# Performance work log

Hardware: AMD Instinct MI355X
Metric: run time of the kernel (lower is better)

The kernel has to match this reference:

```python
import jax, jax.numpy as jnp
import numpy as np

TEMPERATURE = 100.0  # exponential-smoothing temperature from __init__ default
ETA = 1.0            # feature/label cost tradeoff


def _cdist(a, b):
    # Euclidean distance matrix [M, N] between rows of a [M, D] and b [N, D]
    sq = (jnp.sum(a * a, axis=1)[:, None]
          + jnp.sum(b * b, axis=1)[None, :]
          - 2.0 * (a @ b.T))
    return jnp.sqrt(jnp.maximum(sq, 1e-12))


def setup_inputs() -> dict:
    key = jax.random.key(0)
    ks = jax.random.split(key, 9)
    B, Nt, Ns, H, Wd, C = 1024, 8192, 8192, 32, 32, 10
    D = H * Wd
    x = jax.random.normal(ks[0], (B, H, Wd), jnp.float32)
    target_features = jax.random.normal(ks[1], (Nt, H, Wd), jnp.float32)
    aligned_source_features = jax.random.normal(ks[2], (Nt, H, Wd), jnp.float32)
    source_features = jax.random.normal(ks[3], (Ns, H, Wd), jnp.float32)
    source_high_dim_labels = jax.random.uniform(ks[4], (Ns, C), jnp.float32)
    aligned_target_labels = jax.random.uniform(ks[5], (Ns, C), jnp.float32)
    source_label_distances = jax.random.uniform(ks[6], (C, C), jnp.float32)
    W = jax.random.normal(ks[7], (D, C), jnp.float32) * 0.02
    b = jnp.zeros((C,), jnp.float32)
    return {
        "x": x,
        "target_features": target_features,
        "aligned_source_features": aligned_source_features,
        "source_features": source_features,
        "source_high_dim_labels": source_high_dim_labels,
        "aligned_target_labels": aligned_target_labels,
        "source_label_distances": source_label_distances,
        "W": W,
        "b": b,
    }


def reference(x, target_features, aligned_source_features, source_features,
              source_high_dim_labels, aligned_target_labels,
              source_label_distances, W, b):
    B = x.shape[0]
    xf = x.reshape(B, -1)                                   # [B, D]
    tf = target_features.reshape(target_features.shape[0], -1)       # [Nt, D]
    asf = aligned_source_features.reshape(aligned_source_features.shape[0], -1)  # [Nt, D]
    sf = source_features.reshape(source_features.shape[0], -1)       # [Ns, D]

    # --- feature transport: target -> source (plain_softmax) ---
    d_feat = _cdist(xf, tf)                                 # [B, Nt]
    w_feat = jax.nn.softmax(-TEMPERATURE * d_feat, axis=1)  # [B, Nt]
    x_src = w_feat @ asf                                    # [B, D] in source space

    # --- source model (linear classifier head -> soft predictions) ---
    preds = jax.nn.softmax(x_src @ W + b, axis=1)           # [B, C]

    # --- label transport: source -> target (plain_softmax) ---
    cost = _cdist(x_src, sf)                                # feature_dists=True: [B, Ns]
    # label_dists=True: cost of moving predicted label mass to each sample's label
    cost = cost + ETA * (preds @ source_label_distances @ source_high_dim_labels.T)
    w_lab = jax.nn.softmax(-TEMPERATURE * cost, axis=1)     # [B, Ns]
    y = w_lab @ aligned_target_labels                       # [B, C] in target label space
    return y
```

## Files before the change

### kernel.cpp

```cpp
#include <hip/hip_runtime.h>
#include <hip/hip_bf16.h>
#include <math.h>

#define B_ROWS 1024
#define NT 8192
#define NS 8192
#define DIM 1024
#define NC 10
#define TEMP 100.0f
#define WCAP 1024
#define CCAP 512
#define LTHR 18.421681f
#define PREP_RPB 8
#define TSTR 132

typedef __bf16 bf16x8 __attribute__((ext_vector_type(8)));
typedef __bf16 bf16x4 __attribute__((ext_vector_type(4)));
typedef float f32x4 __attribute__((ext_vector_type(4)));

#define GLOAD_LDS(g, l) \
    __builtin_amdgcn_global_load_lds((__attribute__((address_space(1))) void*)(g), \
                                     (__attribute__((address_space(3))) void*)(l), 16, 0, 0)

__device__ inline __bf16 split_hi(float v) { return (__bf16)v; }
__device__ inline __bf16 split_lo(float v) {
    __bf16 h = (__bf16)v;
    return (__bf16)(v - (float)h);
}

__device__ inline float wave_max(float v) {
    #pragma unroll
    for (int off = 32; off > 0; off >>= 1)
        v = fmaxf(v, __shfl_down(v, off, 64));
    return v;
}
__device__ inline float wave_sum(float v) {
    #pragma unroll
    for (int off = 32; off > 0; off >>= 1)
        v += __shfl_down(v, off, 64);
    return v;
}
__device__ inline float max4(float4 v) {
    return fmaxf(fmaxf(v.x, v.y), fmaxf(v.z, v.w));
}

__global__ __launch_bounds__(256) void k_prep0(const float* __restrict__ x,
                                               const float* __restrict__ tf,
                                               const float* __restrict__ sf,
                                               const float* __restrict__ sld,
                                               const float* __restrict__ shdl,
                                               const float* __restrict__ atl,
                                               __bf16* __restrict__ x2,
                                               __bf16* __restrict__ tf2,
                                               __bf16* __restrict__ sf2,
                                               float* __restrict__ nx_,
                                               float* __restrict__ nt_,
                                               float* __restrict__ ns_,
                                               float* __restrict__ M2Tt,
                                               float* __restrict__ atlt,
                                               int* __restrict__ cnt) {
    __shared__ float sred[4][PREP_RPB];
    __shared__ float sldL[NC * NC];
    const int NXB = B_ROWS / PREP_RPB;
    const int NTB = NT / PREP_RPB;
    const int NSB = NS / PREP_RPB;
    int b = blockIdx.x;
    int tid = threadIdx.x;
    if (b < NXB + NTB + NSB) {
        const float* Xp; __bf16* X2p; float* np; int r0;
        if (b < NXB)            { Xp = x;  X2p = x2;  np = nx_; r0 = b * PREP_RPB; }
        else if (b < NXB + NTB) { Xp = tf; X2p = tf2; np = nt_; r0 = (b - NXB) * PREP_RPB; }
        else                    { Xp = sf; X2p = sf2; np = ns_; r0 = (b - NXB - NTB) * PREP_RPB; }
        int c = tid * 4;
        int lane = tid & 63, wid = tid >> 6;
        #pragma unroll
        for (int r = 0; r < PREP_RPB; r++) {
            float4 v = *(const float4*)(Xp + (size_t)(r0 + r) * DIM + c);
            bf16x4 h, l;
            h[0] = split_hi(v.x); l[0] = split_lo(v.x);
            h[1] = split_hi(v.y); l[1] = split_lo(v.y);
            h[2] = split_hi(v.z); l[2] = split_lo(v.z);
            h[3] = split_hi(v.w); l[3] = split_lo(v.w);
            *(bf16x4*)(X2p + (size_t)(r0 + r) * 2048 + c) = h;
            *(bf16x4*)(X2p + (size_t)(r0 + r) * 2048 + 1024 + c) = l;
            float acc = v.x * v.x + v.y * v.y + v.z * v.z + v.w * v.w;
            float w = wave_sum(acc);
            if (lane == 0) sred[wid][r] = w;
        }
        __syncthreads();
        if (tid < PREP_RPB)
            np[r0 + tid] = sred[0][tid] + sred[1][tid] + sred[2][tid] + sred[3][tid];
    } else {
        if (b == NXB + NTB + NSB) {
            #pragma unroll
            for (int z = 0; z < 4; z++) cnt[tid + z * 256] = 0;
        }
        if (tid < NC * NC) sldL[tid] = sld[tid];
        __syncthreads();
        int j = (b - NXB - NTB - NSB) * 256 + tid;
        float sh[NC], at[NC];
        #pragma unroll
        for (int k = 0; k < NC; k++) sh[k] = shdl[(size_t)j * NC + k];
        #pragma unroll
        for (int c = 0; c < NC; c++) at[c] = atl[(size_t)j * NC + c];
        #pragma unroll
        for (int c = 0; c < NC; c++) {
            float t = 0.f;
            #pragma unroll
            for (int k = 0; k < NC; k++) t += sldL[c * NC + k] * sh[k];
            M2Tt[c * NS + j] = t;
            atlt[c * NS + j] = at[c];
        }
    }
}


__global__ __launch_bounds__(512, 4) void k_gemm3L(const __bf16* __restrict__ A2,
                                                   const __bf16* __restrict__ B2,
                                                   float* __restrict__ C,
                                                   int N, int K,
                                                   const float* __restrict__ rowN,
                                                   const float* __restrict__ colN) {
    __shared__ unsigned short AhS[8192], AlS[8192], BhS[8192], BlS[8192];
    __shared__ float extraL[256];
    float* rnL = extraL;
    float* cnL = extraL + 128;

    int tid = threadIdx.x;
    int wid = tid >> 6, lane = tid & 63;
    int wm = (wid >> 2) * 64, wn = (wid & 3) * 32;
    int id = blockIdx.y * gridDim.x + blockIdx.x;
    int bn_i = ((id >> 6) << 3) | (id & 7);
    int bm_i = (id >> 3) & 7;
    int bm = bm_i * 128, bn = bn_i * 128;
    size_t K2 = 2 * (size_t)K;
    int nsteps = K >> 6;

    if (tid < 128) rnL[tid] = rowN[bm + tid];
    else if (tid < 256) cnL[tid - 128] = colN[bn + tid - 128];

    f32x4 acc[4][2];
    #pragma unroll
    for (int i = 0; i < 4; i++)
        #pragma unroll
        for (int j = 0; j < 2; j++) acc[i][j] = (f32x4){0.f, 0.f, 0.f, 0.f};

    int arr = wid & 3, hh = wid >> 2;
    char* arrB = (arr == 0) ? (char*)AhS : (arr == 1) ? (char*)AlS
               : (arr == 2) ? (char*)BhS : (char*)BlS;
    const __bf16* gbase = (arr < 2) ? A2 : B2;
    int rbase = (arr < 2) ? bm : bn;
    int hilo = (arr & 1) ? K : 0;
    int r_in = lane >> 3;
    int cgo = ((lane & 7) ^ r_in) * 8;
    const __bf16* gw = gbase + (size_t)(rbase + hh * 64 + r_in) * K2 + hilo + cgo;
    int ldst = hh * 8192;
    size_t row8 = 8 * K2;

    int ra = lane & 15, q = lane >> 4;
    int aoff[4][2], boff[2][2];
    #pragma unroll
    for (int kh = 0; kh < 2; kh++) {
        #pragma unroll
        for (int i = 0; i < 4; i++) {
            int chunk = ((kh << 2) | q) ^ (ra & 7);
            aoff[i][kh] = (wm + i * 16 + ra) * 64 + chunk * 8;
        }
        #pragma unroll
        for (int j = 0; j < 2; j++) {
            int chunk = ((kh << 2) | q) ^ (ra & 7);
            boff[j][kh] = (wn + j * 16 + ra) * 64 + chunk * 8;
        }
    }
    const __bf16* AhE = (const __bf16*)AhS;
    const __bf16* AlE = (const __bf16*)AlS;
    const __bf16* BhE = (const __bf16*)BhS;
    const __bf16* BlE = (const __bf16*)BlS;

    for (int ks = 0; ks < nsteps; ks++) {
        __syncthreads();
        #pragma unroll
        for (int p = 0; p < 8; p++)
            GLOAD_LDS(gw + (size_t)p * row8, arrB + ldst + p * 1024);
        gw += 64;
        __syncthreads();
        #pragma unroll
        for (int kh = 0; kh < 2; kh++) {
            bf16x8 ah[4], al[4];
            #pragma unroll
            for (int mi = 0; mi < 4; mi++) {
                ah[mi] = *(const bf16x8*)(AhE + aoff[mi][kh]);
                al[mi] = *(const bf16x8*)(AlE + aoff[mi][kh]);
            }
            #pragma unroll
            for (int ni = 0; ni < 2; ni++) {
                bf16x8 bh = *(const bf16x8*)(BhE + boff[ni][kh]);
                bf16x8 bl = *(const bf16x8*)(BlE + boff[ni][kh]);
                #pragma unroll
                for (int mi = 0; mi < 4; mi++) {
                    acc[mi][ni] = __builtin_amdgcn_mfma_f32_16x16x32_bf16(ah[mi], bh, acc[mi][ni], 0, 0, 0);
                    acc[mi][ni] = __builtin_amdgcn_mfma_f32_16x16x32_bf16(ah[mi], bl, acc[mi][ni], 0, 0, 0);
                    acc[mi][ni] = __builtin_amdgcn_mfma_f32_16x16x32_bf16(al[mi], bh, acc[mi][ni], 0, 0, 0);
                }
            }
        }
    }

    #pragma unroll
    for (int mi = 0; mi < 4; mi++) {
        #pragma unroll
        for (int ni = 0; ni < 2; ni++) {
            int cl = wn + ni * 16 + ra;
            float cn = cnL[cl];
            #pragma unroll
            for (int i = 0; i < 4; i++) {
                int rl = wm + mi * 16 + q * 4 + i;
                float sq = rnL[rl] + cn - 2.f * acc[mi][ni][i];
                float d = sqrtf(fmaxf(sq, 1e-12f));
                C[(size_t)(bm + rl) * N + bn + cl] = -TEMP * d;
            }
        }
    }
}

__global__ __launch_bounds__(512, 4) void k_gemm_part(const __bf16* __restrict__ A2,
                                                      const __bf16* __restrict__ B2,
                                                      int N, int K,
                                                      const float* __restrict__ rowN,
                                                      const float* __restrict__ colN,
                                                      float2* __restrict__ ms,
                                                      int* __restrict__ cnt,
                                                      int* __restrict__ candj,
                                                      float* __restrict__ candl) {
    __shared__ union {
        struct { unsigned short Ah[8192], Al[8192], Bh[8192], Bl[8192]; } st;
        float tile[128 * TSTR];
    } U;
    __shared__ float extraL[256];
    float* rnL = extraL;
    float* cnL = extraL + 128;

    int tid = threadIdx.x;
    int wid = tid >> 6, lane = tid & 63;
    int wm = (wid >> 2) * 64, wn = (wid & 3) * 32;
    int id = blockIdx.y * gridDim.x + blockIdx.x;
    int bn_i = ((id >> 6) << 3) | (id & 7);
    int bm_i = (id >> 3) & 7;
    int bm = bm_i * 128, bn = bn_i * 128;
    size_t K2 = 2 * (size_t)K;
    int nsteps = K >> 6;

    if (tid < 128) rnL[tid] = rowN[bm + tid];
    else if (tid < 256) cnL[tid - 128] = colN[bn + tid - 128];

    f32x4 acc[4][2];
    #pragma unroll
    for (int i = 0; i < 4; i++)
        #pragma unroll
        for (int j = 0; j < 2; j++) acc[i][j] = (f32x4){0.f, 0.f, 0.f, 0.f};

    int arr = wid & 3, hh = wid >> 2;
    char* arrB = (arr == 0) ? (char*)U.st.Ah : (arr == 1) ? (char*)U.st.Al
               : (arr == 2) ? (char*)U.st.Bh : (char*)U.st.Bl;
    const __bf16* gbase = (arr < 2) ? A2 : B2;
    int rbase = (arr < 2) ? bm : bn;
    int hilo = (arr & 1) ? K : 0;
    int r_in = lane >> 3;
    int cgo = ((lane & 7) ^ r_in) * 8;
    const __bf16* gw = gbase + (size_t)(rbase + hh * 64 + r_in) * K2 + hilo + cgo;
    int ldst = hh * 8192;
    size_t row8 = 8 * K2;

    int ra = lane & 15, q = lane >> 4;
    int aoff[4][2], boff[2][2];
    #pragma unroll
    for (int kh = 0; kh < 2; kh++) {
        #pragma unroll
        for (int i = 0; i < 4; i++) {
            int chunk = ((kh << 2) | q) ^ (ra & 7);
            aoff[i][kh] = (wm + i * 16 + ra) * 64 + chunk * 8;
        }
        #pragma unroll
        for (int j = 0; j < 2; j++) {
            int chunk = ((kh << 2) | q) ^ (ra & 7);
            boff[j][kh] = (wn + j * 16 + ra) * 64 + chunk * 8;
        }
    }
    const __bf16* AhE = (const __bf16*)U.st.Ah;
    const __bf16* AlE = (const __bf16*)U.st.Al;
    const __bf16* BhE = (const __bf16*)U.st.Bh;
    const __bf16* BlE = (const __bf16*)U.st.Bl;

    for (int ks = 0; ks < nsteps; ks++) {
        __syncthreads();
        #pragma unroll
        for (int p = 0; p < 8; p++)
            GLOAD_LDS(gw + (size_t)p * row8, arrB + ldst + p * 1024);
        gw += 64;
        __syncthreads();
        #pragma unroll
        for (int kh = 0; kh < 2; kh++) {
            bf16x8 ah[4], al[4];
            #pragma unroll
            for (int mi = 0; mi < 4; mi++) {
                ah[mi] = *(const bf16x8*)(AhE + aoff[mi][kh]);
                al[mi] = *(const bf16x8*)(AlE + aoff[mi][kh]);
            }
            #pragma unroll
            for (int ni = 0; ni < 2; ni++) {
                bf16x8 bh = *(const bf16x8*)(BhE + boff[ni][kh]);
                bf16x8 bl = *(const bf16x8*)(BlE + boff[ni][kh]);
                #pragma unroll
                for (int mi = 0; mi < 4; mi++) {
                    acc[mi][ni] = __builtin_amdgcn_mfma_f32_16x16x32_bf16(ah[mi], bh, acc[mi][ni], 0, 0, 0);
                    acc[mi][ni] = __builtin_amdgcn_mfma_f32_16x16x32_bf16(ah[mi], bl, acc[mi][ni], 0, 0, 0);
                    acc[mi][ni] = __builtin_amdgcn_mfma_f32_16x16x32_bf16(al[mi], bh, acc[mi][ni], 0, 0, 0);
                }
            }
        }
    }

    __syncthreads();
    #pragma unroll
    for (int mi = 0; mi < 4; mi++) {
        #pragma unroll
        for (int ni = 0; ni < 2; ni++) {
            int cl = wn + ni * 16 + ra;
            float cn = cnL[cl];
            #pragma unroll
            for (int i = 0; i < 4; i++) {
                int rl = wm + mi * 16 + q * 4 + i;
                float sq = rnL[rl] + cn - 2.f * acc[mi][ni][i];
                U.tile[rl * TSTR + cl] = -TEMP * sqrtf(fmaxf(sq, 1e-12f));
            }
        }
    }
    __syncthreads();

    int r = tid >> 2, qt = tid & 3;
    const float4* rowp = (const float4*)&U.tile[r * TSTR + qt * 32];
    float4 v[8];
    float m = -1e30f;
    #pragma unroll
    for (int k = 0; k < 8; k++) {
        v[k] = rowp[k];
        m = fmaxf(m, max4(v[k]));
    }
    m = fmaxf(m, __shfl_xor(m, 1, 64));
    m = fmaxf(m, __shfl_xor(m, 2, 64));
    float s = 0.f;
    #pragma unroll
    for (int k = 0; k < 8; k++) {
        s += __expf(v[k].x - m) + __expf(v[k].y - m)
           + __expf(v[k].z - m) + __expf(v[k].w - m);
    }
    s += __shfl_xor(s, 1, 64);
    s += __shfl_xor(s, 2, 64);
    int gr = bm + r;
    if (qt == 0) ms[(size_t)gr * 64 + bn_i] = make_float2(m, s);
    float thr = m - LTHR;
    #pragma unroll
    for (int k = 0; k < 8; k++) {
        #pragma unroll
        for (int e = 0; e < 4; e++) {
            float lv = (e == 0) ? v[k].x : (e == 1) ? v[k].y : (e == 2) ? v[k].z : v[k].w;
            if (lv > thr) {
                int kk = atomicAdd(&cnt[gr], 1);
                if (kk < CCAP) {
                    candj[(size_t)gr * CCAP + kk] = bn + qt * 32 + k * 4 + e;
                    candl[(size_t)gr * CCAP + kk] = lv;
                }
            }
        }
    }
}

__global__ __launch_bounds__(256) void k_xsrc(const float2* __restrict__ ms,
                                              const int* __restrict__ cnt,
                                              const int* __restrict__ candj,
                                              const float* __restrict__ candl,
                                              const float* __restrict__ asf,
                                              const float* __restrict__ W,
                                              const float* __restrict__ bias,
                                              __bf16* __restrict__ xsrc2,
                                              float* __restrict__ nx2_,
                                              float* __restrict__ preds) {
    __shared__ float sm[4];
    __shared__ float ss[4];
    __shared__ int   sidx[WCAP];
    __shared__ float swt[WCAP];
    __shared__ int   scnt;
    __shared__ float red[4][NC + 1];
    int row = blockIdx.x;
    int tid = threadIdx.x;
    int lane = tid & 63, wid = tid >> 6;
    if (tid == 0) scnt = 0;
    float2 msv = ms[(size_t)row * 64 + lane];
    float wmx = wave_max(msv.x);
    if (lane == 0) sm[wid] = wmx;
    __syncthreads();
    float M = fmaxf(fmaxf(sm[0], sm[1]), fmaxf(sm[2], sm[3]));
    float sp = msv.y * __expf(msv.x - M);
    float wsv = wave_sum(sp);
    if (lane == 0) ss[wid] = wsv;
    __syncthreads();
    float inv = 1.0f / ss[0];
    int n = cnt[row]; n = n < CCAP ? n : CCAP;
    for (int i = tid; i < n; i += 256) {
        float w = __expf(candl[(size_t)row * CCAP + i] - M) * inv;
        if (w > 1e-8f) {
            int k = atomicAdd(&scnt, 1);
            if (k < WCAP) { sidx[k] = candj[(size_t)row * CCAP + i]; swt[k] = w; }
        }
    }
    __syncthreads();
    int cw = scnt < WCAP ? scnt : WCAP;
    int c = tid * 4;
    float sx = 0.f, sy = 0.f, sz = 0.f, sw = 0.f;
    for (int i = 0; i < cw; i++) {
        float wg = swt[i];
        float4 v = *(const float4*)(asf + (size_t)sidx[i] * DIM + c);
        sx += wg * v.x; sy += wg * v.y; sz += wg * v.z; sw += wg * v.w;
    }
    bf16x4 h, l;
    h[0] = split_hi(sx); l[0] = split_lo(sx);
    h[1] = split_hi(sy); l[1] = split_lo(sy);
    h[2] = split_hi(sz); l[2] = split_lo(sz);
    h[3] = split_hi(sw); l[3] = split_lo(sw);
    *(bf16x4*)(xsrc2 + (size_t)row * 2048 + c) = h;
    *(bf16x4*)(xsrc2 + (size_t)row * 2048 + 1024 + c) = l;
    float accn = sx * sx + sy * sy + sz * sz + sw * sw;
    float accp[NC];
    #pragma unroll
    for (int cc = 0; cc < NC; cc++)
        accp[cc] = sx * W[(c + 0) * NC + cc] + sy * W[(c + 1) * NC + cc]
                 + sz * W[(c + 2) * NC + cc] + sw * W[(c + 3) * NC + cc];
    accn = wave_sum(accn);
    #pragma unroll
    for (int cc = 0; cc < NC; cc++) accp[cc] = wave_sum(accp[cc]);
    if (lane == 0) {
        red[wid][0] = accn;
        #pragma unroll
        for (int cc = 0; cc < NC; cc++) red[wid][1 + cc] = accp[cc];
    }
    __syncthreads();
    if (tid == 0) {
        nx2_[row] = red[0][0] + red[1][0] + red[2][0] + red[3][0];
        float lo[NC];
        float m = -1e30f;
        #pragma unroll
        for (int cc = 0; cc < NC; cc++) {
            lo[cc] = red[0][1 + cc] + red[1][1 + cc] + red[2][1 + cc] + red[3][1 + cc]
                   + bias[cc];
            m = fmaxf(m, lo[cc]);
        }
        float ssum = 0.f;
        #pragma unroll
        for (int cc = 0; cc < NC; cc++) {
            lo[cc] = __expf(lo[cc] - m);
            ssum += lo[cc];
        }
        float iv = 1.0f / ssum;
        #pragma unroll
        for (int cc = 0; cc < NC; cc++) preds[(size_t)row * NC + cc] = lo[cc] * iv;
    }
}

__global__ __launch_bounds__(256) void k_lab_softmax_y(const float* __restrict__ S,
                                                       const float* __restrict__ predsG,
                                                       const float* __restrict__ M2Tt,
                                                       const float* __restrict__ atlt,
                                                       float* __restrict__ y) {
    int r0 = blockIdx.x * 2, r1 = r0 + 1;
    float pr0[NC], pr1[NC];
    #pragma unroll
    for (int c = 0; c < NC; c++) {
        pr0[c] = TEMP * predsG[(size_t)r0 * NC + c];
        pr1[c] = TEMP * predsG[(size_t)r1 * NC + c];
    }
    const float4* s0 = (const float4*)(S + (size_t)r0 * NS);
    const float4* s1 = (const float4*)(S + (size_t)r1 * NS);
    const float4* M2 = (const float4*)M2Tt;
    const float4* AT = (const float4*)atlt;
    float4 v0[NS / 1024], v1[NS / 1024];
    float m0 = -1e30f, m1 = -1e30f;
    #pragma unroll
    for (int u = 0; u < NS / 1024; u++) {
        int j4 = threadIdx.x + u * 256;
        float4 a = s0[j4], b = s1[j4];
        float4 lab0 = make_float4(0.f, 0.f, 0.f, 0.f);
        float4 lab1 = make_float4(0.f, 0.f, 0.f, 0.f);
        #pragma unroll
        for (int c = 0; c < NC; c++) {
            float4 mv = M2[c * 2048 + j4];
            lab0.x += pr0[c] * mv.x; lab0.y += pr0[c] * mv.y;
            lab0.z += pr0[c] * mv.z; lab0.w += pr0[c] * mv.w;
            lab1.x += pr1[c] * mv.x; lab1.y += pr1[c] * mv.y;
            lab1.z += pr1[c] * mv.z; lab1.w += pr1[c] * mv.w;
        }
        a.x -= lab0.x; a.y -= lab0.y;
        a.z -= lab0.z; a.w -= lab0.w;
        b.x -= lab1.x; b.y -= lab1.y;
        b.z -= lab1.z; b.w -= lab1.w;
        v0[u] = a; v1[u] = b;
        m0 = fmaxf(m0, fmaxf(fmaxf(a.x, a.y), fmaxf(a.z, a.w)));
        m1 = fmaxf(m1, fmaxf(fmaxf(b.x, b.y), fmaxf(b.z, b.w)));
    }
    __shared__ float sm[2][4];
    __shared__ float ss[2][4];
    __shared__ float yred[4][2][NC];
    int lane = threadIdx.x & 63, wid = threadIdx.x >> 6;
    float wm0 = wave_max(m0), wm1 = wave_max(m1);
    if (lane == 0) { sm[0][wid] = wm0; sm[1][wid] = wm1; }
    __syncthreads();
    float bm0 = fmaxf(fmaxf(sm[0][0], sm[0][1]), fmaxf(sm[0][2], sm[0][3]));
    float bm1 = fmaxf(fmaxf(sm[1][0], sm[1][1]), fmaxf(sm[1][2], sm[1][3]));
    float ls0 = 0.f, ls1 = 0.f;
    #pragma unroll
    for (int u = 0; u < NS / 1024; u++) {
        float4 a = v0[u], b = v1[u];
        a.x = __expf(a.x - bm0); a.y = __expf(a.y - bm0);
        a.z = __expf(a.z - bm0); a.w = __expf(a.w - bm0);
        b.x = __expf(b.x - bm1); b.y = __expf(b.y - bm1);
        b.z = __expf(b.z - bm1); b.w = __expf(b.w - bm1);
        v0[u] = a; v1[u] = b;
        ls0 += a.x + a.y + a.z + a.w;
        ls1 += b.x + b.y + b.z + b.w;
    }
    float ws0 = wave_sum(ls0), ws1 = wave_sum(ls1);
    if (lane == 0) { ss[0][wid] = ws0; ss[1][wid] = ws1; }
    __syncthreads();
    float inv0 = 1.0f / (ss[0][0] + ss[0][1] + ss[0][2] + ss[0][3]);
    float inv1 = 1.0f / (ss[1][0] + ss[1][1] + ss[1][2] + ss[1][3]);
    float y0[NC] = {}, y1[NC] = {};
    #pragma unroll
    for (int u = 0; u < NS / 1024; u++) {
        int j4 = threadIdx.x + u * 256;
        float4 a = v0[u], b = v1[u];
        #pragma unroll
        for (int c = 0; c < NC; c++) {
            float4 av = AT[c * 2048 + j4];
            y0[c] += a.x * av.x + a.y * av.y + a.z * av.z + a.w * av.w;
            y1[c] += b.x * av.x + b.y * av.y + b.z * av.z + b.w * av.w;
        }
    }
    #pragma unroll
    for (int c = 0; c < NC; c++) {
        y0[c] = wave_sum(y0[c]) * inv0;
        y1[c] = wave_sum(y1[c]) * inv1;
    }
    if (lane == 0) {
        #pragma unroll
        for (int c = 0; c < NC; c++) { yred[wid][0][c] = y0[c]; yred[wid][1][c] = y1[c]; }
    }
    __syncthreads();
    if (threadIdx.x < 2 * NC) {
        int r = threadIdx.x / NC, c = threadIdx.x - r * NC;
        y[(size_t)(r0 + r) * NC + c] = yred[0][r][c] + yred[1][r][c] + yred[2][r][c] + yred[3][r][c];
    }
}

extern "C" void kernel_launch(void* const* d_in, const int* in_sizes, int n_in,
                              void* d_out, int out_size, void* d_ws, size_t ws_size,
                              hipStream_t stream) {
    const float* x    = (const float*)d_in[0];
    const float* tf   = (const float*)d_in[1];
    const float* asf  = (const float*)d_in[2];
    const float* sf   = (const float*)d_in[3];
    const float* shdl = (const float*)d_in[4];
    const float* atl  = (const float*)d_in[5];
    const float* sld  = (const float*)d_in[6];
    const float* W    = (const float*)d_in[7];
    const float* bias = (const float*)d_in[8];
    float* y = (float*)d_out;

    char* wsb = (char*)d_ws;
    int*    candj = (int*)(wsb);
    float*  candl = (float*)(wsb + (2u << 20));
    float2* ms    = (float2*)(wsb + (4u << 20));
    int*    cnt   = (int*)(wsb + (4u << 20) + (512u << 10));
    float*  S     = (float*)(wsb);
    __bf16* tf2   = (__bf16*)(wsb + (32u << 20));
    __bf16* sf2   = (__bf16*)(wsb + (64u << 20));
    __bf16* x2    = (__bf16*)(wsb + (96u << 20));
    __bf16* xsrc2 = (__bf16*)(wsb + (100u << 20));
    float*  nt_   = (float*)(wsb + (108u << 20));
    float*  ns_   = nt_ + NT;
    float*  nx_   = ns_ + NS;
    float*  nx2_  = nx_ + B_ROWS;
    float*  preds = nx2_ + B_ROWS;
    float*  M2Tt  = preds + B_ROWS * NC;
    float*  atlt  = M2Tt + NS * NC;

    {
        int nblk = B_ROWS / PREP_RPB + NT / PREP_RPB + NS / PREP_RPB + NS / 256;
        k_prep0<<<nblk, 256, 0, stream>>>(x, tf, sf, sld, shdl, atl,
                                          x2, tf2, sf2, nx_, nt_, ns_, M2Tt, atlt,
                                          cnt);
    }

    {
        dim3 g(NT / 128, B_ROWS / 128, 1);
        k_gemm_part<<<g, 512, 0, stream>>>(x2, tf2, NT, DIM, nx_, nt_,
                                           ms, cnt, candj, candl);
    }

    k_xsrc<<<B_ROWS, 256, 0, stream>>>(ms, cnt, candj, candl, asf, W, bias,
                                       xsrc2, nx2_, preds);

    {
        dim3 g(NS / 128, B_ROWS / 128, 1);
        k_gemm3L<<<g, 512, 0, stream>>>(xsrc2, sf2, S, NS, DIM, nx2_, ns_);
    }
    k_lab_softmax_y<<<B_ROWS / 2, 256, 0, stream>>>(S, preds, M2Tt, atlt, y);
}
```

Before: 284.1 us.

## Fuse label softmax and label transport into the second distance GEMM epilogue

The separate label-softmax kernel goes away, and the full [B, Ns] score matrix is no longer written to or read back from global memory. Each GEMM tile now stages its scores in shared memory, adds the label cost, and computes a per-tile partial softmax (max, sum, weighted label sums). These partials go to a small buffer, and the last block for each row group, found with an atomic counter, merges them into the output. This removes a 32MB round trip and one launch, at the cost of a longer GEMM epilogue and an atomic/threadfence tail.

```diff
diff --git a/kernel.cpp b/kernel.cpp
--- a/kernel.cpp
+++ b/kernel.cpp
@@ -58,7 +58,8 @@
                                                float* __restrict__ ns_,
                                                float* __restrict__ M2Tt,
                                                float* __restrict__ atlt,
-                                               int* __restrict__ cnt) {
+                                               int* __restrict__ cnt,
+                                               int* __restrict__ done2) {
     __shared__ float sred[4][PREP_RPB];
     __shared__ float sldL[NC * NC];
     const int NXB = B_ROWS / PREP_RPB;
@@ -94,6 +95,7 @@
         if (b == NXB + NTB + NSB) {
             #pragma unroll
             for (int z = 0; z < 4; z++) cnt[tid + z * 256] = 0;
+            if (tid < 8) done2[tid] = 0;
         }
         if (tid < NC * NC) sldL[tid] = sld[tid];
         __syncthreads();
@@ -110,115 +112,6 @@
             for (int k = 0; k < NC; k++) t += sldL[c * NC + k] * sh[k];
             M2Tt[c * NS + j] = t;
             atlt[c * NS + j] = at[c];
-        }
-    }
-}
-
-
-__global__ __launch_bounds__(512, 4) void k_gemm3L(const __bf16* __restrict__ A2,
-                                                   const __bf16* __restrict__ B2,
-                                                   float* __restrict__ C,
-                                                   int N, int K,
-                                                   const float* __restrict__ rowN,
-                                                   const float* __restrict__ colN) {
-    __shared__ unsigned short AhS[8192], AlS[8192], BhS[8192], BlS[8192];
-    __shared__ float extraL[256];
-    float* rnL = extraL;
-    float* cnL = extraL + 128;
-
-    int tid = threadIdx.x;
-    int wid = tid >> 6, lane = tid & 63;
-    int wm = (wid >> 2) * 64, wn = (wid & 3) * 32;
-    int id = blockIdx.y * gridDim.x + blockIdx.x;
-    int bn_i = ((id >> 6) << 3) | (id & 7);
-    int bm_i = (id >> 3) & 7;
-    int bm = bm_i * 128, bn = bn_i * 128;
-    size_t K2 = 2 * (size_t)K;
-    int nsteps = K >> 6;
-
-    if (tid < 128) rnL[tid] = rowN[bm + tid];
-    else if (tid < 256) cnL[tid - 128] = colN[bn + tid - 128];
-
-    f32x4 acc[4][2];
-    #pragma unroll
-    for (int i = 0; i < 4; i++)
-        #pragma unroll
-        for (int j = 0; j < 2; j++) acc[i][j] = (f32x4){0.f, 0.f, 0.f, 0.f};
-
-    int arr = wid & 3, hh = wid >> 2;
-    char* arrB = (arr == 0) ? (char*)AhS : (arr == 1) ? (char*)AlS
-               : (arr == 2) ? (char*)BhS : (char*)BlS;
-    const __bf16* gbase = (arr < 2) ? A2 : B2;
-    int rbase = (arr < 2) ? bm : bn;
-    int hilo = (arr & 1) ? K : 0;
-    int r_in = lane >> 3;
-    int cgo = ((lane & 7) ^ r_in) * 8;
-    const __bf16* gw = gbase + (size_t)(rbase + hh * 64 + r_in) * K2 + hilo + cgo;
-    int ldst = hh * 8192;
-    size_t row8 = 8 * K2;
-
-    int ra = lane & 15, q = lane >> 4;
-    int aoff[4][2], boff[2][2];
-    #pragma unroll
-    for (int kh = 0; kh < 2; kh++) {
-        #pragma unroll
-        for (int i = 0; i < 4; i++) {
-            int chunk = ((kh << 2) | q) ^ (ra & 7);
-            aoff[i][kh] = (wm + i * 16 + ra) * 64 + chunk * 8;
-        }
-        #pragma unroll
-        for (int j = 0; j < 2; j++) {
-            int chunk = ((kh << 2) | q) ^ (ra & 7);
-            boff[j][kh] = (wn + j * 16 + ra) * 64 + chunk * 8;
-        }
-    }
-    const __bf16* AhE = (const __bf16*)AhS;
-    const __bf16* AlE = (const __bf16*)AlS;
-    const __bf16* BhE = (const __bf16*)BhS;
-    const __bf16* BlE = (const __bf16*)BlS;
-
-    for (int ks = 0; ks < nsteps; ks++) {
-        __syncthreads();
-        #pragma unroll
-        for (int p = 0; p < 8; p++)
-            GLOAD_LDS(gw + (size_t)p * row8, arrB + ldst + p * 1024);
-        gw += 64;
-        __syncthreads();
-        #pragma unroll
-        for (int kh = 0; kh < 2; kh++) {
-            bf16x8 ah[4], al[4];
-            #pragma unroll
-            for (int mi = 0; mi < 4; mi++) {
-                ah[mi] = *(const bf16x8*)(AhE + aoff[mi][kh]);
-                al[mi] = *(const bf16x8*)(AlE + aoff[mi][kh]);
-            }
-            #pragma unroll
-            for (int ni = 0; ni < 2; ni++) {
-                bf16x8 bh = *(const bf16x8*)(BhE + boff[ni][kh]);
-                bf16x8 bl = *(const bf16x8*)(BlE + boff[ni][kh]);
-                #pragma unroll
-                for (int mi = 0; mi < 4; mi++) {
-                    acc[mi][ni] = __builtin_amdgcn_mfma_f32_16x16x32_bf16(ah[mi], bh, acc[mi][ni], 0, 0, 0);
-                    acc[mi][ni] = __builtin_amdgcn_mfma_f32_16x16x32_bf16(ah[mi], bl, acc[mi][ni], 0, 0, 0);
-                    acc[mi][ni] = __builtin_amdgcn_mfma_f32_16x16x32_bf16(al[mi], bh, acc[mi][ni], 0, 0, 0);
-                }
-            }
-        }
-    }
-
-    #pragma unroll
-    for (int mi = 0; mi < 4; mi++) {
-        #pragma unroll
-        for (int ni = 0; ni < 2; ni++) {
-            int cl = wn + ni * 16 + ra;
-            float cn = cnL[cl];
-            #pragma unroll
-            for (int i = 0; i < 4; i++) {
-                int rl = wm + mi * 16 + q * 4 + i;
-                float sq = rnL[rl] + cn - 2.f * acc[mi][ni][i];
-                float d = sqrtf(fmaxf(sq, 1e-12f));
-                C[(size_t)(bm + rl) * N + bn + cl] = -TEMP * d;
-            }
         }
     }
 }
@@ -466,97 +359,215 @@
     }
 }
 
-__global__ __launch_bounds__(256) void k_lab_softmax_y(const float* __restrict__ S,
-                                                       const float* __restrict__ predsG,
-                                                       const float* __restrict__ M2Tt,
-                                                       const float* __restrict__ atlt,
-                                                       float* __restrict__ y) {
-    int r0 = blockIdx.x * 2, r1 = r0 + 1;
-    float pr0[NC], pr1[NC];
-    #pragma unroll
-    for (int c = 0; c < NC; c++) {
-        pr0[c] = TEMP * predsG[(size_t)r0 * NC + c];
-        pr1[c] = TEMP * predsG[(size_t)r1 * NC + c];
-    }
-    const float4* s0 = (const float4*)(S + (size_t)r0 * NS);
-    const float4* s1 = (const float4*)(S + (size_t)r1 * NS);
+__global__ __launch_bounds__(512, 4) void k_gemm3Y(const __bf16* __restrict__ A2,
+                                                   const __bf16* __restrict__ B2,
+                                                   int N, int K,
+                                                   const float* __restrict__ rowN,
+                                                   const float* __restrict__ colN,
+                                                   const float* __restrict__ predsG,
+                                                   const float* __restrict__ M2Tt,
+                                                   const float* __restrict__ atlt,
+                                                   float* __restrict__ P,
+                                                   int* __restrict__ done2,
+                                                   float* __restrict__ y) {
+    __shared__ union {
+        struct { unsigned short Ah[8192], Al[8192], Bh[8192], Bl[8192]; } st;
+        float tile[128 * TSTR];
+    } U;
+    __shared__ float extraL[256];
+    __shared__ int lastF;
+    float* rnL = extraL;
+    float* cnL = extraL + 128;
+
+    int tid = threadIdx.x;
+    int wid = tid >> 6, lane = tid & 63;
+    int wm = (wid >> 2) * 64, wn = (wid & 3) * 32;
+    int id = blockIdx.y * gridDim.x + blockIdx.x;
+    int bn_i = ((id >> 6) << 3) | (id & 7);
+    int bm_i = (id >> 3) & 7;
+    int bm = bm_i * 128, bn = bn_i * 128;
+    size_t K2 = 2 * (size_t)K;
+    int nsteps = K >> 6;
+
+    if (tid < 128) rnL[tid] = rowN[bm + tid];
+    else if (tid < 256) cnL[tid - 128] = colN[bn + tid - 128];
+
+    f32x4 acc[4][2];
+    #pragma unroll
+    for (int i = 0; i < 4; i++)
+        #pragma unroll
+        for (int j = 0; j < 2; j++) acc[i][j] = (f32x4){0.f, 0.f, 0.f, 0.f};
+
+    int arr = wid & 3, hh = wid >> 2;
+    char* arrB = (arr == 0) ? (char*)U.st.Ah : (arr == 1) ? (char*)U.st.Al
+               : (arr == 2) ? (char*)U.st.Bh : (char*)U.st.Bl;
+    const __bf16* gbase = (arr < 2) ? A2 : B2;
+    int rbase = (arr < 2) ? bm : bn;
+    int hilo = (arr & 1) ? K : 0;
+    int r_in = lane >> 3;
+    int cgo = ((lane & 7) ^ r_in) * 8;
+    const __bf16* gw = gbase + (size_t)(rbase + hh * 64 + r_in) * K2 + hilo + cgo;
+    int ldst = hh * 8192;
+    size_t row8 = 8 * K2;
+
+    int ra = lane & 15, q = lane >> 4;
+    int aoff[4][2], boff[2][2];
+    #pragma unroll
+    for (int kh = 0; kh < 2; kh++) {
+        #pragma unroll
+        for (int i = 0; i < 4; i++) {
+            int chunk = ((kh << 2) | q) ^ (ra & 7);
+            aoff[i][kh] = (wm + i * 16 + ra) * 64 + chunk * 8;
+        }
+        #pragma unroll
+        for (int j = 0; j < 2; j++) {
+            int chunk = ((kh << 2) | q) ^ (ra & 7);
+            boff[j][kh] = (wn + j * 16 + ra) * 64 + chunk * 8;
+        }
+    }
+    const __bf16* AhE = (const __bf16*)U.st.Ah;
+    const __bf16* AlE = (const __bf16*)U.st.Al;
+    const __bf16* BhE = (const __bf16*)U.st.Bh;
+    const __bf16* BlE = (const __bf16*)U.st.Bl;
+
+    for (int ks = 0; ks < nsteps; ks++) {
+        __syncthreads();
+        #pragma unroll
+        for (int p = 0; p < 8; p++)
+            GLOAD_LDS(gw + (size_t)p * row8, arrB + ldst + p * 1024);
+        gw += 64;
+        __syncthreads();
+        #pragma unroll
+        for (int kh = 0; kh < 2; kh++) {
+            bf16x8 ah[4], al[4];
+            #pragma unroll
+            for (int mi = 0; mi < 4; mi++) {
+                ah[mi] = *(const bf16x8*)(AhE + aoff[mi][kh]);
+                al[mi] = *(const bf16x8*)(AlE + aoff[mi][kh]);
+            }
+            #pragma unroll
+            for (int ni = 0; ni < 2; ni++) {
+                bf16x8 bh = *(const bf16x8*)(BhE + boff[ni][kh]);
+                bf16x8 bl = *(const bf16x8*)(BlE + boff[ni][kh]);
+                #pragma unroll
+                for (int mi = 0; mi < 4; mi++) {
+                    acc[mi][ni] = __builtin_amdgcn_mfma_f32_16x16x32_bf16(ah[mi], bh, acc[mi][ni], 0, 0, 0);
+                    acc[mi][ni] = __builtin_amdgcn_mfma_f32_16x16x32_bf16(ah[mi], bl, acc[mi][ni], 0, 0, 0);
+                    acc[mi][ni] = __builtin_amdgcn_mfma_f32_16x16x32_bf16(al[mi], bh, acc[mi][ni], 0, 0, 0);
+                }
+            }
+        }
+    }
+
+    __syncthreads();
+    #pragma unroll
+    for (int mi = 0; mi < 4; mi++) {
+        #pragma unroll
+        for (int ni = 0; ni < 2; ni++) {
+            int cl = wn + ni * 16 + ra;
+            float cn = cnL[cl];
+            #pragma unroll
+            for (int i = 0; i < 4; i++) {
+                int rl = wm + mi * 16 + q * 4 + i;
+                float sq = rnL[rl] + cn - 2.f * acc[mi][ni][i];
+                U.tile[rl * TSTR + cl] = -TEMP * sqrtf(fmaxf(sq, 1e-12f));
+            }
+        }
+    }
+    __syncthreads();
+
+    int r = tid >> 2, qt = tid & 3;
+    int gr = bm + r;
+    float pr[NC];
+    #pragma unroll
+    for (int c = 0; c < NC; c++) pr[c] = TEMP * predsG[(size_t)gr * NC + c];
     const float4* M2 = (const float4*)M2Tt;
     const float4* AT = (const float4*)atlt;
-    float4 v0[NS / 1024], v1[NS / 1024];
-    float m0 = -1e30f, m1 = -1e30f;
-    #pragma unroll
-    for (int u = 0; u < NS / 1024; u++) {
-        int j4 = threadIdx.x + u * 256;
-        float4 a = s0[j4], b = s1[j4];
-        float4 lab0 = make_float4(0.f, 0.f, 0.f, 0.f);
-        float4 lab1 = make_float4(0.f, 0.f, 0.f, 0.f);
+    int cb = (bn >> 2) + qt * 8;
+    const float4* rowp = (const float4*)&U.tile[r * TSTR + qt * 32];
+    float4 v[8];
+    float m = -1e30f;
+    #pragma unroll
+    for (int k = 0; k < 8; k++) {
+        float4 sv = rowp[k];
+        float4 lab = make_float4(0.f, 0.f, 0.f, 0.f);
         #pragma unroll
         for (int c = 0; c < NC; c++) {
-            float4 mv = M2[c * 2048 + j4];
-            lab0.x += pr0[c] * mv.x; lab0.y += pr0[c] * mv.y;
-            lab0.z += pr0[c] * mv.z; lab0.w += pr0[c] * mv.w;
-            lab1.x += pr1[c] * mv.x; lab1.y += pr1[c] * mv.y;
-            lab1.z += pr1[c] * mv.z; lab1.w += pr1[c] * mv.w;
-        }
-        a.x -= lab0.x; a.y -= lab0.y;
-        a.z -= lab0.z; a.w -= lab0.w;
-        b.x -= lab1.x; b.y -= lab1.y;
-        b.z -= lab1.z; b.w -= lab1.w;
-        v0[u] = a; v1[u] = b;
-        m0 = fmaxf(m0, fmaxf(fmaxf(a.x, a.y), fmaxf(a.z, a.w)));
-        m1 = fmaxf(m1, fmaxf(fmaxf(b.x, b.y), fmaxf(b.z, b.w)));
-    }
-    __shared__ float sm[2][4];
-    __shared__ float ss[2][4];
-    __shared__ float yred[4][2][NC];
-    int lane = threadIdx.x & 63, wid = threadIdx.x >> 6;
-    float wm0 = wave_max(m0), wm1 = wave_max(m1);
-    if (lane == 0) { sm[0][wid] = wm0; sm[1][wid] = wm1; }
-    __syncthreads();
-    float bm0 = fmaxf(fmaxf(sm[0][0], sm[0][1]), fmaxf(sm[0][2], sm[0][3]));
-    float bm1 = fmaxf(fmaxf(sm[1][0], sm[1][1]), fmaxf(sm[1][2], sm[1][3]));
-    float ls0 = 0.f, ls1 = 0.f;
-    #pragma unroll
-    for (int u = 0; u < NS / 1024; u++) {
-        float4 a = v0[u], b = v1[u];
-        a.x = __expf(a.x - bm0); a.y = __expf(a.y - bm0);
-        a.z = __expf(a.z - bm0); a.w = __expf(a.w - bm0);
-        b.x = __expf(b.x - bm1); b.y = __expf(b.y - bm1);
-        b.z = __expf(b.z - bm1); b.w = __expf(b.w - bm1);
-        v0[u] = a; v1[u] = b;
-        ls0 += a.x + a.y + a.z + a.w;
-        ls1 += b.x + b.y + b.z + b.w;
-    }
-    float ws0 = wave_sum(ls0), ws1 = wave_sum(ls1);
-    if (lane == 0) { ss[0][wid] = ws0; ss[1][wid] = ws1; }
-    __syncthreads();
-    float inv0 = 1.0f / (ss[0][0] + ss[0][1] + ss[0][2] + ss[0][3]);
-    float inv1 = 1.0f / (ss[1][0] + ss[1][1] + ss[1][2] + ss[1][3]);
-    float y0[NC] = {}, y1[NC] = {};
-    #pragma unroll
-    for (int u = 0; u < NS / 1024; u++) {
-        int j4 = threadIdx.x + u * 256;
-        float4 a = v0[u], b = v1[u];
+            float4 mv = M2[(c << 11) + cb + k];
+            lab.x += pr[c] * mv.x; lab.y += pr[c] * mv.y;
+            lab.z += pr[c] * mv.z; lab.w += pr[c] * mv.w;
+        }
+        sv.x -= lab.x; sv.y -= lab.y; sv.z -= lab.z; sv.w -= lab.w;
+        v[k] = sv;
+        m = fmaxf(m, max4(sv));
+    }
+    m = fmaxf(m, __shfl_xor(m, 1, 64));
+    m = fmaxf(m, __shfl_xor(m, 2, 64));
+    float s = 0.f;
+    float Y[NC] = {};
+    #pragma unroll
+    for (int k = 0; k < 8; k++) {
+        float4 p;
+        p.x = __expf(v[k].x - m); p.y = __expf(v[k].y - m);
+        p.z = __expf(v[k].z - m); p.w = __expf(v[k].w - m);
+        s += p.x + p.y + p.z + p.w;
         #pragma unroll
         for (int c = 0; c < NC; c++) {
-            float4 av = AT[c * 2048 + j4];
-            y0[c] += a.x * av.x + a.y * av.y + a.z * av.z + a.w * av.w;
-            y1[c] += b.x * av.x + b.y * av.y + b.z * av.z + b.w * av.w;
-        }
-    }
+            float4 av = AT[(c << 11) + cb + k];
+            Y[c] += p.x * av.x + p.y * av.y + p.z * av.z + p.w * av.w;
+        }
+    }
+    s += __shfl_xor(s, 1, 64);
+    s += __shfl_xor(s, 2, 64);
     #pragma unroll
     for (int c = 0; c < NC; c++) {
-        y0[c] = wave_sum(y0[c]) * inv0;
-        y1[c] = wave_sum(y1[c]) * inv1;
-    }
-    if (lane == 0) {
-        #pragma unroll
-        for (int c = 0; c < NC; c++) { yred[wid][0][c] = y0[c]; yred[wid][1][c] = y1[c]; }
-    }
-    __syncthreads();
-    if (threadIdx.x < 2 * NC) {
-        int r = threadIdx.x / NC, c = threadIdx.x - r * NC;
-        y[(size_t)(r0 + r) * NC + c] = yred[0][r][c] + yred[1][r][c] + yred[2][r][c] + yred[3][r][c];
+        Y[c] += __shfl_xor(Y[c], 1, 64);
+        Y[c] += __shfl_xor(Y[c], 2, 64);
+    }
+    if (qt == 0) {
+        float* Pp = P + ((size_t)gr * 64 + bn_i) * 12;
+        Pp[0] = m; Pp[1] = s;
+        #pragma unroll
+        for (int c = 0; c < NC; c++) Pp[2 + c] = Y[c];
+    }
+
+    __syncthreads();
+    if (tid == 0) {
+        __threadfence();
+        int old = atomicAdd(&done2[bm_i], 1);
+        lastF = (old == 63);
+    }
+    __syncthreads();
+    if (!lastF) return;
+    __threadfence();
+
+    float mm = -1e30f;
+    #pragma unroll
+    for (int b = 0; b < 16; b++)
+        mm = fmaxf(mm, P[((size_t)gr * 64 + qt * 16 + b) * 12]);
+    mm = fmaxf(mm, __shfl_xor(mm, 1, 64));
+    mm = fmaxf(mm, __shfl_xor(mm, 2, 64));
+    float den = 0.f;
+    float y10[NC] = {};
+    #pragma unroll
+    for (int b = 0; b < 16; b++) {
+        const float* Pp = P + ((size_t)gr * 64 + qt * 16 + b) * 12;
+        float e = __expf(Pp[0] - mm);
+        den += Pp[1] * e;
+        #pragma unroll
+        for (int c = 0; c < NC; c++) y10[c] += Pp[2 + c] * e;
+    }
+    den += __shfl_xor(den, 1, 64);
+    den += __shfl_xor(den, 2, 64);
+    #pragma unroll
+    for (int c = 0; c < NC; c++) {
+        y10[c] += __shfl_xor(y10[c], 1, 64);
+        y10[c] += __shfl_xor(y10[c], 2, 64);
+    }
+    if (qt == 0) {
+        float invd = 1.0f / den;
+        #pragma unroll
+        for (int c = 0; c < NC; c++) y[(size_t)gr * NC + c] = y10[c] * invd;
     }
 }
 
@@ -579,7 +590,8 @@
     float*  candl = (float*)(wsb + (2u << 20));
     float2* ms    = (float2*)(wsb + (4u << 20));
     int*    cnt   = (int*)(wsb + (4u << 20) + (512u << 10));
-    float*  S     = (float*)(wsb);
+    int*    done2 = cnt + B_ROWS;
+    float*  P     = (float*)(wsb + (8u << 20));
     __bf16* tf2   = (__bf16*)(wsb + (32u << 20));
     __bf16* sf2   = (__bf16*)(wsb + (64u << 20));
     __bf16* x2    = (__bf16*)(wsb + (96u << 20));
@@ -596,7 +608,7 @@
         int nblk = B_ROWS / PREP_RPB + NT / PREP_RPB + NS / PREP_RPB + NS / 256;
         k_prep0<<<nblk, 256, 0, stream>>>(x, tf, sf, sld, shdl, atl,
                                           x2, tf2, sf2, nx_, nt_, ns_, M2Tt, atlt,
-                                          cnt);
+                                          cnt, done2);
     }
 
     {
@@ -610,7 +622,7 @@
 
     {
         dim3 g(NS / 128, B_ROWS / 128, 1);
-        k_gemm3L<<<g, 512, 0, stream>>>(xsrc2, sf2, S, NS, DIM, nx2_, ns_);
-    }
-    k_lab_softmax_y<<<B_ROWS / 2, 256, 0, stream>>>(S, preds, M2Tt, atlt, y);
-}
+        k_gemm3Y<<<g, 512, 0, stream>>>(xsrc2, sf2, NS, DIM, nx2_, ns_,
+                                        preds, M2Tt, atlt, P, done2, y);
+    }
+}
```

Result: slower. 368.9 us (+29.9%).
